# Kernel optimization log

Hardware: AMD Instinct MI355X
Metric: run time of the kernel (lower is better)

Reference implementation:

```python
import jax, jax.numpy as jnp
import numpy as np

B, S, D, H = 2, 2048, 1024, 16
DH = D // H
SCALE = 1.0 / float(np.sqrt(DH))


def setup_inputs() -> dict:
    key = jax.random.key(0)
    ks = jax.random.split(key, 5)
    x = jax.random.normal(ks[0], (B, S, D), dtype=jnp.float32)
    init = 0.02
    Wq = jax.random.normal(ks[1], (D, D), dtype=jnp.float32) * init
    Wk = jax.random.normal(ks[2], (D, D), dtype=jnp.float32) * init
    Wv = jax.random.normal(ks[3], (D, D), dtype=jnp.float32) * init
    Wo = jax.random.normal(ks[4], (D, D), dtype=jnp.float32) * init
    bq = jnp.zeros((D,), dtype=jnp.float32)
    bk = jnp.zeros((D,), dtype=jnp.float32)
    bv = jnp.zeros((D,), dtype=jnp.float32)
    bo = jnp.zeros((D,), dtype=jnp.float32)
    return {"x": x, "Wq": Wq, "bq": bq, "Wk": Wk, "bk": bk,
            "Wv": Wv, "bv": bv, "Wo": Wo, "bo": bo}


def reference(x, Wq, bq, Wk, bk, Wv, bv, Wo, bo):
    # torch Linear: y = x @ W.T + b  (W: [out, in])
    q = x @ Wq.T + bq  # [B,S,D]
    k = x @ Wk.T + bk
    v = x @ Wv.T + bv
    # split heads -> [B,H,S,dh]
    q = q.reshape(B, S, H, DH).transpose(0, 2, 1, 3)
    k = k.reshape(B, S, H, DH).transpose(0, 2, 1, 3)
    v = v.reshape(B, S, H, DH).transpose(0, 2, 1, 3)
    scores = jnp.einsum('bhqd,bhkd->bhqk', q, k) * SCALE  # [B,H,S,S]
    p = jax.nn.softmax(scores, axis=-1)
    o = jnp.einsum('bhqk,bhkd->bhqd', p, v)  # [B,H,S,dh]
    # faithful to original: view(B, d_model, S) then transpose(-1,-2)
    o = o.reshape(B, D, S).swapaxes(-1, -2)  # [B,S,D]
    return o @ Wo.T + bo
```

## Files before the change

kernel.cpp:

```cpp
#include <hip/hip_runtime.h>
#include <cstdint>
#include <cstddef>


typedef _Float16 h16;
typedef _Float16 h16x8 __attribute__((ext_vector_type(8)));
typedef _Float16 h16x4 __attribute__((ext_vector_type(4)));
typedef float    f32x4 __attribute__((ext_vector_type(4)));
typedef unsigned int u32x4 __attribute__((ext_vector_type(4)));

#define MFMA16 __builtin_amdgcn_mfma_f32_16x16x32_f16

#define QSCALE 0.1803368801111204f

#if __has_builtin(__builtin_amdgcn_exp2f)
#define EXP2F(x) __builtin_amdgcn_exp2f(x)
#else
#define EXP2F(x) exp2f(x)
#endif

__device__ __forceinline__ void gload_lds16(char* lds_dst, const void* gsrc) {
  __builtin_amdgcn_global_load_lds(
      (__attribute__((address_space(1))) void*)gsrc,
      (__attribute__((address_space(3))) void*)lds_dst,
      16, 0, 0);
}

__device__ __forceinline__ unsigned pk2(float lo, float hi) {
  return __builtin_bit_cast(unsigned, __builtin_amdgcn_cvt_pkrtz(lo, hi));
}

__device__ __forceinline__ void swap32(unsigned& a, unsigned& b) {
  asm("v_permlane32_swap_b32 %0, %1" : "+v"(a), "+v"(b));
}

__device__ __forceinline__ h16x8 mk8(unsigned u0, unsigned u1, unsigned u2, unsigned u3) {
  u32x4 v = {u0, u1, u2, u3};
  return __builtin_bit_cast(h16x8, v);
}


__global__ __launch_bounds__(256)
void cast_all(const float* __restrict__ x,
              const float* __restrict__ wq, const float* __restrict__ wk,
              const float* __restrict__ wv, const float* __restrict__ wo,
              h16* __restrict__ xb, h16* __restrict__ wqb, h16* __restrict__ wkb,
              h16* __restrict__ wvb, h16* __restrict__ wob) {
  const int z = blockIdx.y;
  const float* src; h16* dst; int n4;
  switch (z) {
    case 0:  src = x;  dst = xb;  n4 = 1048576; break;
    case 1:  src = wq; dst = wqb; n4 = 262144;  break;
    case 2:  src = wk; dst = wkb; n4 = 262144;  break;
    case 3:  src = wv; dst = wvb; n4 = 262144;  break;
    default: src = wo; dst = wob; n4 = 262144;  break;
  }
  int i = blockIdx.x * 256 + threadIdx.x;
  const int stride = gridDim.x * 256;
  for (; i < n4; i += stride) {
    float4 v = reinterpret_cast<const float4*>(src)[i];
    h16x4 o = { (h16)v.x, (h16)v.y, (h16)v.z, (h16)v.w };
    reinterpret_cast<h16x4*>(dst)[i] = o;
  }
}

__device__ __forceinline__ void gemm_core_128(
    const h16* __restrict__ A, const h16* __restrict__ W,
    char* lds, f32x4 (&acc)[4][4])
{
  const int tid  = threadIdx.x;
  const int lane = tid & 63;
  const int w    = tid >> 6;
  const int wr   = w >> 1, wc = w & 1;
  const int blockRow = blockIdx.y * 128;
  const int blockCol = blockIdx.x * 128;

  const int sr  = (tid >> 2) & 15;
  const int sc  = tid & 3;
  const int skc = sc ^ ((sr >> 1) & 3);

  const h16* srcA0 = A + (size_t)(blockRow + (0 * 4 + w) * 16 + sr) * 1024 + skc * 8;
  const h16* srcA1 = A + (size_t)(blockRow + (1 * 4 + w) * 16 + sr) * 1024 + skc * 8;
  const h16* srcB0 = W + (size_t)(blockCol + (0 * 4 + w) * 16 + sr) * 1024 + skc * 8;
  const h16* srcB1 = W + (size_t)(blockCol + (1 * 4 + w) * 16 + sr) * 1024 + skc * 8;

  const int dA0o = w * 1024;
  const int dA1o = 4096 + w * 1024;
  const int dB0o = 8192 + w * 1024;
  const int dB1o = 12288 + w * 1024;

  const int fr = lane & 15, fg = lane >> 4;
  const int foff = fr * 64 + ((fg ^ ((fr >> 1) & 3)) << 4);

#pragma unroll
  for (int i = 0; i < 4; ++i)
#pragma unroll
    for (int j = 0; j < 4; ++j) acc[i][j] = f32x4{0.f, 0.f, 0.f, 0.f};

  gload_lds16(lds + dA0o, srcA0);
  gload_lds16(lds + dA1o, srcA1);
  gload_lds16(lds + dB0o, srcB0);
  gload_lds16(lds + dB1o, srcB1);

  for (int ks = 0; ks < 32; ++ks) {
    char* buf = lds + (ks & 1) * 16384;
    __syncthreads();
    if (ks != 31) {
      char* nbuf = lds + ((ks & 1) ^ 1) * 16384;
      gload_lds16(nbuf + dA0o, srcA0 + (ks + 1) * 32);
      gload_lds16(nbuf + dA1o, srcA1 + (ks + 1) * 32);
      gload_lds16(nbuf + dB0o, srcB0 + (ks + 1) * 32);
      gload_lds16(nbuf + dB1o, srcB1 + (ks + 1) * 32);
    }
    char* ldsA = buf;
    char* ldsB = buf + 8192;

    h16x8 af[4], bfv[4];
#pragma unroll
    for (int t = 0; t < 4; ++t)
      af[t] = *(const h16x8*)(ldsA + (wr * 4 + t) * 1024 + foff);
#pragma unroll
    for (int t = 0; t < 4; ++t)
      bfv[t] = *(const h16x8*)(ldsB + (wc * 4 + t) * 1024 + foff);
#pragma unroll
    for (int i = 0; i < 4; ++i)
#pragma unroll
      for (int j = 0; j < 4; ++j)
        acc[i][j] = MFMA16(af[i], bfv[j], acc[i][j], 0, 0, 0);
  }
}

__global__ __launch_bounds__(256, 2)
void gemm_qkv(const h16* __restrict__ xb,
              const h16* __restrict__ wq, const h16* __restrict__ wk, const h16* __restrict__ wv,
              const float* __restrict__ bq, const float* __restrict__ bk, const float* __restrict__ bv,
              h16* __restrict__ q_, h16* __restrict__ k_, h16* __restrict__ vt_)
{
  __shared__ alignas(128) char lds[32768];
  const int z = blockIdx.z;
  const h16* W = (z == 0) ? wq : (z == 1) ? wk : wv;
  const float* bias = (z == 0) ? bq : (z == 1) ? bk : bv;

  f32x4 acc[4][4];
  gemm_core_128(xb, W, lds, acc);

  const int lane = threadIdx.x & 63;
  const int w = threadIdx.x >> 6;
  const int wr = w >> 1, wc = w & 1;
  const int fr = lane & 15, fg = lane >> 4;
  const int blockRow = blockIdx.y * 128;
  const int blockCol = blockIdx.x * 128;

  if (z == 2) {
#pragma unroll
    for (int ct = 0; ct < 4; ++ct) {
      int n = blockCol + wc * 64 + ct * 16 + fr;
      int hh = n >> 6, dd = n & 63;
      float bv_ = bias[n];
#pragma unroll
      for (int rt = 0; rt < 4; ++rt) {
        int m = blockRow + wr * 64 + rt * 16 + 4 * fg;
        int bb = m >> 11, s0 = m & 2047;
        h16x4 pack = { (h16)(acc[rt][ct][0] + bv_), (h16)(acc[rt][ct][1] + bv_),
                       (h16)(acc[rt][ct][2] + bv_), (h16)(acc[rt][ct][3] + bv_) };
        *(h16x4*)(vt_ + ((size_t)((bb * 16 + hh) * 64 + dd)) * 2048 + s0) = pack;
      }
    }
  } else {
    const float scl = (z == 0) ? QSCALE : 1.0f;
    h16* dst = (z == 0) ? q_ : k_;
#pragma unroll
    for (int ct = 0; ct < 4; ++ct) {
      int n = blockCol + wc * 64 + ct * 16 + fr;
      float bv_ = bias[n];
#pragma unroll
      for (int rt = 0; rt < 4; ++rt) {
        int m0 = blockRow + wr * 64 + rt * 16 + 4 * fg;
#pragma unroll
        for (int r = 0; r < 4; ++r)
          dst[(size_t)(m0 + r) * 1024 + n] = (h16)((acc[rt][ct][r] + bv_) * scl);
      }
    }
  }
}

__global__ __launch_bounds__(256, 2)
void gemm_out(const h16* __restrict__ yt, const h16* __restrict__ wo,
              const float* __restrict__ bo, float* __restrict__ out)
{
  __shared__ alignas(128) char lds[32768];
  f32x4 acc[4][4];
  gemm_core_128(yt, wo, lds, acc);

  const int lane = threadIdx.x & 63;
  const int w = threadIdx.x >> 6;
  const int wr = w >> 1, wc = w & 1;
  const int fr = lane & 15, fg = lane >> 4;
  const int blockRow = blockIdx.y * 128;
  const int blockCol = blockIdx.x * 128;

#pragma unroll
  for (int ct = 0; ct < 4; ++ct) {
    int n = blockCol + wc * 64 + ct * 16 + fr;
    float bv_ = bo[n];
#pragma unroll
    for (int rt = 0; rt < 4; ++rt) {
      int m0 = blockRow + wr * 64 + rt * 16 + 4 * fg;
#pragma unroll
      for (int r = 0; r < 4; ++r)
        out[(size_t)(m0 + r) * 1024 + n] = acc[rt][ct][r] + bv_;
    }
  }
}

__global__ __launch_bounds__(256, 1)
void attn_kernel(const h16* __restrict__ qb, const h16* __restrict__ kb,
                 const h16* __restrict__ vtb, h16* __restrict__ ytb)
{
  __shared__ alignas(128) char lds[32768];
  const int tid = threadIdx.x, lane = tid & 63, w = tid >> 6;
  const int fr = lane & 15, fg = lane >> 4;

  const int orig = blockIdx.x;
  const int wgid = (orig & 7) * 32 + (orig >> 3);
  const int p  = wgid & 7;
  const int hh = (wgid >> 3) & 15;
  const int b  = wgid >> 7;

  const int aq = w * 16 + fr;
  const h16* qrow0 = qb + ((size_t)(b * 2048 + 32 * aq + p)) * 1024 + hh * 64;
  h16x8 qf[4][2];
#pragma unroll
  for (int X = 0; X < 4; ++X) {
    qf[X][0] = *(const h16x8*)(qrow0 + (size_t)(8 * X) * 1024 + fg * 8);
    qf[X][1] = *(const h16x8*)(qrow0 + (size_t)(8 * X) * 1024 + 32 + fg * 8);
  }

  const int sr  = (tid >> 2) & 15;
  const int sc  = tid & 3;
  const int skc = sc ^ ((sr >> 1) & 3);
  const int rloc0 = (w >> 1) * 16 + sr;
  const int rloc1 = ((4 + w) >> 1) * 16 + sr;
  const int kc0 = (w & 1) * 32 + skc * 8;
  const int kc1 = ((4 + w) & 1) * 32 + skc * 8;

  const h16* srcK0 = kb + ((size_t)(b * 2048 + rloc0)) * 1024 + hh * 64 + kc0;
  const h16* srcK1 = kb + ((size_t)(b * 2048 + rloc1)) * 1024 + hh * 64 + kc1;
  const h16* srcV0 = vtb + ((size_t)((b * 16 + hh) * 64 + rloc0)) * 2048 + kc0;
  const h16* srcV1 = vtb + ((size_t)((b * 16 + hh) * 64 + rloc1)) * 2048 + kc1;

  const int dK0o = w * 1024, dK1o = 4096 + w * 1024;
  const int dV0o = 8192 + w * 1024, dV1o = 12288 + w * 1024;

  const int foff = fr * 64 + ((fg ^ ((fr >> 1) & 3)) << 4);
  const int sfr  = (fr & 3) | ((fr & 4) << 1) | ((fr & 8) >> 1);
  const int foffK = sfr * 64 + ((fg ^ ((sfr >> 1) & 3)) << 4);

  const h16x8 ones8 = { (h16)1.f, (h16)1.f, (h16)1.f, (h16)1.f,
                        (h16)1.f, (h16)1.f, (h16)1.f, (h16)1.f };

  f32x4 o[4][4];
  f32x4 l4[4];
#pragma unroll
  for (int X = 0; X < 4; ++X) {
    l4[X] = f32x4{0.f,0.f,0.f,0.f};
#pragma unroll
    for (int dt = 0; dt < 4; ++dt) o[X][dt] = f32x4{0.f,0.f,0.f,0.f};
  }

  gload_lds16(lds + dK0o, srcK0);
  gload_lds16(lds + dK1o, srcK1);
  gload_lds16(lds + dV0o, srcV0);
  gload_lds16(lds + dV1o, srcV1);

  for (int ch = 0; ch < 32; ++ch) {
    char* buf = lds + (ch & 1) * 16384;
    __syncthreads();
    if (ch != 31) {
      char* nbuf = lds + ((ch & 1) ^ 1) * 16384;
      gload_lds16(nbuf + dK0o, srcK0 + (size_t)(ch + 1) * 65536);
      gload_lds16(nbuf + dK1o, srcK1 + (size_t)(ch + 1) * 65536);
      gload_lds16(nbuf + dV0o, srcV0 + (size_t)(ch + 1) * 64);
      gload_lds16(nbuf + dV1o, srcV1 + (size_t)(ch + 1) * 64);
    }
    char* ldsK = buf;
    char* ldsV = buf + 8192;

    unsigned pp[4][4][2];
#pragma unroll
    for (int t = 0; t < 4; ++t) {
      h16x8 kf0 = *(const h16x8*)(ldsK + (t * 2 + 0) * 1024 + foffK);
      h16x8 kf1 = *(const h16x8*)(ldsK + (t * 2 + 1) * 1024 + foffK);
      f32x4 s[4];
      __builtin_amdgcn_s_setprio(1);
#pragma unroll
      for (int X = 0; X < 4; ++X) {
        s[X] = f32x4{0.f,0.f,0.f,0.f};
        s[X] = MFMA16(kf0, qf[X][0], s[X], 0, 0, 0);
        s[X] = MFMA16(kf1, qf[X][1], s[X], 0, 0, 0);
      }
      __builtin_amdgcn_s_setprio(0);
#pragma unroll
      for (int X = 0; X < 4; ++X) {
        pp[X][t][0] = pk2(EXP2F(s[X][0]), EXP2F(s[X][1]));
        pp[X][t][1] = pk2(EXP2F(s[X][2]), EXP2F(s[X][3]));
      }
    }

    h16x8 pf[4][2];
#pragma unroll
    for (int X = 0; X < 4; ++X) {
      swap32(pp[X][0][0], pp[X][1][0]);  swap32(pp[X][0][1], pp[X][1][1]);
      swap32(pp[X][2][0], pp[X][3][0]);  swap32(pp[X][2][1], pp[X][3][1]);
      pf[X][0] = mk8(pp[X][0][0], pp[X][0][1], pp[X][1][0], pp[X][1][1]);
      pf[X][1] = mk8(pp[X][2][0], pp[X][2][1], pp[X][3][0], pp[X][3][1]);
    }

    __builtin_amdgcn_s_setprio(1);
#pragma unroll
    for (int X = 0; X < 4; ++X) {
      l4[X] = MFMA16(pf[X][0], ones8, l4[X], 0, 0, 0);
      l4[X] = MFMA16(pf[X][1], ones8, l4[X], 0, 0, 0);
    }
#pragma unroll
    for (int dt = 0; dt < 4; ++dt) {
      h16x8 vf0 = *(const h16x8*)(ldsV + (dt * 2 + 0) * 1024 + foff);
      h16x8 vf1 = *(const h16x8*)(ldsV + (dt * 2 + 1) * 1024 + foff);
#pragma unroll
      for (int X = 0; X < 4; ++X) {
        o[X][dt] = MFMA16(pf[X][0], vf0, o[X][dt], 0, 0, 0);
        o[X][dt] = MFMA16(pf[X][1], vf1, o[X][dt], 0, 0, 0);
      }
    }
    __builtin_amdgcn_s_setprio(0);
  }

  f32x4 i4[4];
#pragma unroll
  for (int X = 0; X < 4; ++X)
#pragma unroll
    for (int r = 0; r < 4; ++r) i4[X][r] = 1.0f / l4[X][r];

#pragma unroll
  for (int X = 0; X < 4; ++X) {
#pragma unroll
    for (int dt = 0; dt < 4; ++dt) {
      int row = dt * 16 + fr;
      size_t colb = (size_t)(hh * 64 + w * 16 + fg * 4);
      h16x4 s4 = { (h16)(o[X][dt][0] * i4[X][0]), (h16)(o[X][dt][1] * i4[X][1]),
                   (h16)(o[X][dt][2] * i4[X][2]), (h16)(o[X][dt][3] * i4[X][3]) };
      *(h16x4*)(ytb + ((size_t)(b * 2048 + (p + 8 * X) * 64 + row)) * 1024 + colb) = s4;
    }
  }
}

extern "C" void kernel_launch(void* const* d_in, const int* in_sizes, int n_in,
                              void* d_out, int out_size, void* d_ws, size_t ws_size,
                              hipStream_t stream) {
  const float* x  = (const float*)d_in[0];
  const float* Wq = (const float*)d_in[1];
  const float* bq = (const float*)d_in[2];
  const float* Wk = (const float*)d_in[3];
  const float* bk = (const float*)d_in[4];
  const float* Wv = (const float*)d_in[5];
  const float* bv = (const float*)d_in[6];
  const float* Wo = (const float*)d_in[7];
  const float* bo = (const float*)d_in[8];

  char* ws = (char*)d_ws;
  h16* xb  = (h16*)(ws);
  h16* wqb = (h16*)(ws + (size_t)(8  << 20));
  h16* wkb = (h16*)(ws + (size_t)(10 << 20));
  h16* wvb = (h16*)(ws + (size_t)(12 << 20));
  h16* wob = (h16*)(ws + (size_t)(14 << 20));
  h16* q_  = (h16*)(ws + (size_t)(16 << 20));
  h16* k_  = (h16*)(ws + (size_t)(24 << 20));
  h16* vt_ = (h16*)(ws + (size_t)(32 << 20));
  h16* yt_ = (h16*)(ws + (size_t)(40 << 20));

  cast_all<<<dim3(512, 5), 256, 0, stream>>>(x, Wq, Wk, Wv, Wo, xb, wqb, wkb, wvb, wob);
  gemm_qkv<<<dim3(8, 32, 3), 256, 0, stream>>>(xb, wqb, wkb, wvb, bq, bk, bv, q_, k_, vt_);
  attn_kernel<<<256, 256, 0, stream>>>(q_, k_, vt_, yt_);
  gemm_out<<<dim3(8, 32, 1), 256, 0, stream>>>(yt_, wob, bo, (float*)d_out);
}
```

Baseline: 118.2 us.

## Split attention over two KV halves and merge partial outputs in a separate kernel

```diff
diff --git a/kernel.cpp b/kernel.cpp
--- a/kernel.cpp
+++ b/kernel.cpp
@@ -130,7 +130,7 @@
   }
 }
 
-__global__ __launch_bounds__(256, 2)
+__global__ __launch_bounds__(256, 3)
 void gemm_qkv(const h16* __restrict__ xb,
               const h16* __restrict__ wq, const h16* __restrict__ wk, const h16* __restrict__ wv,
               const float* __restrict__ bq, const float* __restrict__ bk, const float* __restrict__ bv,
@@ -184,7 +184,7 @@
   }
 }
 
-__global__ __launch_bounds__(256, 2)
+__global__ __launch_bounds__(256, 3)
 void gemm_out(const h16* __restrict__ yt, const h16* __restrict__ wo,
               const float* __restrict__ bo, float* __restrict__ out)
 {
@@ -213,19 +213,26 @@
   }
 }
 
-__global__ __launch_bounds__(256, 1)
+__global__ __launch_bounds__(256, 2)
 void attn_kernel(const h16* __restrict__ qb, const h16* __restrict__ kb,
-                 const h16* __restrict__ vtb, h16* __restrict__ ytb)
+                 const h16* __restrict__ vtb,
+                 h16* __restrict__ o1, h16* __restrict__ o2,
+                 float* __restrict__ l1, float* __restrict__ l2)
 {
   __shared__ alignas(128) char lds[32768];
   const int tid = threadIdx.x, lane = tid & 63, w = tid >> 6;
   const int fr = lane & 15, fg = lane >> 4;
 
   const int orig = blockIdx.x;
-  const int wgid = (orig & 7) * 32 + (orig >> 3);
-  const int p  = wgid & 7;
-  const int hh = (wgid >> 3) & 15;
-  const int b  = wgid >> 7;
+  const int wgid = (orig & 7) * 64 + (orig >> 3);
+  const int half = wgid & 1;
+  const int p    = (wgid >> 1) & 7;
+  const int hh   = (wgid >> 4) & 15;
+  const int b    = wgid >> 8;
+  const int kvb  = half * 1024;
+
+  h16* __restrict__ oP = half ? o2 : o1;
+  float* __restrict__ lP = half ? l2 : l1;
 
   const int aq = w * 16 + fr;
   const h16* qrow0 = qb + ((size_t)(b * 2048 + 32 * aq + p)) * 1024 + hh * 64;
@@ -244,10 +251,10 @@
   const int kc0 = (w & 1) * 32 + skc * 8;
   const int kc1 = ((4 + w) & 1) * 32 + skc * 8;
 
-  const h16* srcK0 = kb + ((size_t)(b * 2048 + rloc0)) * 1024 + hh * 64 + kc0;
-  const h16* srcK1 = kb + ((size_t)(b * 2048 + rloc1)) * 1024 + hh * 64 + kc1;
-  const h16* srcV0 = vtb + ((size_t)((b * 16 + hh) * 64 + rloc0)) * 2048 + kc0;
-  const h16* srcV1 = vtb + ((size_t)((b * 16 + hh) * 64 + rloc1)) * 2048 + kc1;
+  const h16* srcK0 = kb + ((size_t)(b * 2048 + kvb + rloc0)) * 1024 + hh * 64 + kc0;
+  const h16* srcK1 = kb + ((size_t)(b * 2048 + kvb + rloc1)) * 1024 + hh * 64 + kc1;
+  const h16* srcV0 = vtb + ((size_t)((b * 16 + hh) * 64 + rloc0)) * 2048 + kvb + kc0;
+  const h16* srcV1 = vtb + ((size_t)((b * 16 + hh) * 64 + rloc1)) * 2048 + kvb + kc1;
 
   const int dK0o = w * 1024, dK1o = 4096 + w * 1024;
   const int dV0o = 8192 + w * 1024, dV1o = 12288 + w * 1024;
@@ -273,10 +280,10 @@
   gload_lds16(lds + dV0o, srcV0);
   gload_lds16(lds + dV1o, srcV1);
 
-  for (int ch = 0; ch < 32; ++ch) {
+  for (int ch = 0; ch < 16; ++ch) {
     char* buf = lds + (ch & 1) * 16384;
     __syncthreads();
-    if (ch != 31) {
+    if (ch != 15) {
       char* nbuf = lds + ((ch & 1) ^ 1) * 16384;
       gload_lds16(nbuf + dK0o, srcK0 + (size_t)(ch + 1) * 65536);
       gload_lds16(nbuf + dK1o, srcK1 + (size_t)(ch + 1) * 65536);
@@ -335,23 +342,56 @@
     __builtin_amdgcn_s_setprio(0);
   }
 
-  f32x4 i4[4];
-#pragma unroll
-  for (int X = 0; X < 4; ++X)
-#pragma unroll
-    for (int r = 0; r < 4; ++r) i4[X][r] = 1.0f / l4[X][r];
-
 #pragma unroll
   for (int X = 0; X < 4; ++X) {
 #pragma unroll
     for (int dt = 0; dt < 4; ++dt) {
       int row = dt * 16 + fr;
       size_t colb = (size_t)(hh * 64 + w * 16 + fg * 4);
-      h16x4 s4 = { (h16)(o[X][dt][0] * i4[X][0]), (h16)(o[X][dt][1] * i4[X][1]),
-                   (h16)(o[X][dt][2] * i4[X][2]), (h16)(o[X][dt][3] * i4[X][3]) };
-      *(h16x4*)(ytb + ((size_t)(b * 2048 + (p + 8 * X) * 64 + row)) * 1024 + colb) = s4;
-    }
-  }
+      h16x4 s4 = { (h16)o[X][dt][0], (h16)o[X][dt][1],
+                   (h16)o[X][dt][2], (h16)o[X][dt][3] };
+      *(h16x4*)(oP + ((size_t)(b * 2048 + (p + 8 * X) * 64 + row)) * 1024 + colb) = s4;
+    }
+  }
+  if (fr == 0) {
+#pragma unroll
+    for (int X = 0; X < 4; ++X) {
+      float* dst = lP + ((size_t)((b * 16 + hh) * 32 + (p + 8 * X))) * 64 + w * 16 + 4 * fg;
+      *(f32x4*)dst = l4[X];
+    }
+  }
+}
+
+__global__ __launch_bounds__(256)
+void merge_halves(const h16* __restrict__ o1, const h16* __restrict__ o2,
+                  const float* __restrict__ l1, const float* __restrict__ l2,
+                  h16* __restrict__ yt)
+{
+  int idx = blockIdx.x * 256 + threadIdx.x;
+  int row  = idx >> 7;
+  int colg = (idx & 127) << 3;
+  int b  = row >> 11;
+  int b2 = (row >> 6) & 31;
+  int h  = colg >> 6;
+  int a0 = colg & 63;
+  const float* L1 = l1 + ((size_t)((b * 16 + h) * 32 + b2)) * 64 + a0;
+  const float* L2 = l2 + ((size_t)((b * 16 + h) * 32 + b2)) * 64 + a0;
+  f32x4 La0 = *(const f32x4*)L1,       La1 = *(const f32x4*)(L1 + 4);
+  f32x4 Lb0 = *(const f32x4*)L2,       Lb1 = *(const f32x4*)(L2 + 4);
+  h16x8 u1 = *(const h16x8*)(o1 + (size_t)row * 1024 + colg);
+  h16x8 u2 = *(const h16x8*)(o2 + (size_t)row * 1024 + colg);
+  h16x8 yv;
+#pragma unroll
+  for (int i = 0; i < 4; ++i) {
+    float inv = 1.0f / (La0[i] + Lb0[i]);
+    yv[i] = (h16)(((float)u1[i] + (float)u2[i]) * inv);
+  }
+#pragma unroll
+  for (int i = 0; i < 4; ++i) {
+    float inv = 1.0f / (La1[i] + Lb1[i]);
+    yv[4 + i] = (h16)(((float)u1[4 + i] + (float)u2[4 + i]) * inv);
+  }
+  *(h16x8*)(yt + (size_t)row * 1024 + colg) = yv;
 }
 
 extern "C" void kernel_launch(void* const* d_in, const int* in_sizes, int n_in,
@@ -376,10 +416,15 @@
   h16* q_  = (h16*)(ws + (size_t)(16 << 20));
   h16* k_  = (h16*)(ws + (size_t)(24 << 20));
   h16* vt_ = (h16*)(ws + (size_t)(32 << 20));
-  h16* yt_ = (h16*)(ws + (size_t)(40 << 20));
+  h16* o1_ = (h16*)(ws + (size_t)(40 << 20));
+  h16* o2_ = (h16*)(ws + (size_t)(48 << 20));
+  float* l1_ = (float*)(ws + (size_t)(56 << 20));
+  float* l2_ = (float*)(ws + (size_t)(56 << 20) + 262144);
+  h16* yt_ = (h16*)(ws);
 
   cast_all<<<dim3(512, 5), 256, 0, stream>>>(x, Wq, Wk, Wv, Wo, xb, wqb, wkb, wvb, wob);
   gemm_qkv<<<dim3(8, 32, 3), 256, 0, stream>>>(xb, wqb, wkb, wvb, bq, bk, bv, q_, k_, vt_);
-  attn_kernel<<<256, 256, 0, stream>>>(q_, k_, vt_, yt_);
+  attn_kernel<<<512, 256, 0, stream>>>(q_, k_, vt_, o1_, o2_, l1_, l2_);
+  merge_halves<<<2048, 256, 0, stream>>>(o1_, o2_, l1_, l2_, yt_);
   gemm_out<<<dim3(8, 32, 1), 256, 0, stream>>>(yt_, wob, bo, (float*)d_out);
 }
```

New measurement: 112.4 us. -4.9%, faster.
